# Kernel optimization log

Measured on AMD Instinct MI355X. Metric: run time of the kernel, lower is better.

Reference implementation:

```python
import jax, jax.numpy as jnp
import numpy as np

B, D, H, W, N = 64, 512, 32, 32, 20
E = 512  # emb_size
TEMP = 10.0


def setup_inputs() -> dict:
    key = jax.random.key(0)
    ks = jax.random.split(key, 16)
    inp = {
        "fvisu": jax.random.normal(ks[0], (B, D, H, W), jnp.float32),
        "fword": jax.random.normal(ks[1], (B, N, D), jnp.float32),
        "context_score": jax.random.uniform(ks[2], (B, N), jnp.float32),
        "fcoord": jax.random.normal(ks[3], (B, 8, H, W), jnp.float32),
        "gest": jax.random.normal(ks[4], (B, 8), jnp.float32),
        "word_mask": jax.random.randint(ks[5], (B, N), 0, 2, jnp.int32),
        # parameters (kaiming-uniform-ish scale)
        "attn_map_w": jax.random.normal(ks[6], (E // 2, D), jnp.float32) * (1.0 / np.sqrt(D)),
        "attn_map_b": jnp.zeros((E // 2,), jnp.float32),
        "attn_score_w": jax.random.normal(ks[7], (1, E // 2), jnp.float32) * (1.0 / np.sqrt(E // 2)),
        "attn_score_b": jnp.zeros((1,), jnp.float32),
        "gamma_w": jax.random.normal(ks[8], (2 * E, D), jnp.float32) * (1.0 / np.sqrt(D)),
        "gamma_b": jnp.zeros((2 * E,), jnp.float32),
        "conv1_w": jax.random.normal(ks[9], (E, D + 8), jnp.float32) * (1.0 / np.sqrt(D + 8)),
        "conv1_b": jnp.zeros((E,), jnp.float32),
    }
    return inp


def mask_softmax(attn_score, word_mask, temp=TEMP):
    # score: (B, N)
    score = jax.nn.softmax(attn_score * temp, axis=1)
    m = word_mask.astype(jnp.int32)
    m = m.at[:, 0].set(0)                      # zero CLS position
    idx = jnp.sum(m, axis=1)                   # index of SEP (post-CLS-zeroing), matches torch loop
    m = m.at[jnp.arange(m.shape[0]), idx].set(0)
    ms = score * m.astype(score.dtype)
    return ms / (jnp.sum(ms, axis=1, keepdims=True) + 1e-8)


def reference(fvisu, fword, context_score, fcoord, gest, word_mask,
              attn_map_w, attn_map_b, attn_score_w, attn_score_b,
              gamma_w, gamma_b, conv1_w, conv1_b):
    # fword: (B, N, D) -> module permutes to (B, D, N)
    fw = jnp.transpose(fword, (0, 2, 1))                      # (B, D, N)
    tile_visu = jnp.mean(fvisu.reshape(B, D, -1), axis=2, keepdims=True)  # (B, D, 1)
    context_tile = tile_visu * fw * context_score[:, None, :]  # (B, D, N)

    # 1x1 Conv1d -> GEMM
    attn_feat = jnp.tanh(jnp.einsum('od,bdn->bon', attn_map_w, context_tile)
                         + attn_map_b[None, :, None])          # (B, E/2, N)
    attn_score = (jnp.einsum('oc,bcn->bon', attn_score_w, attn_feat)[:, 0, :]
                  + attn_score_b[0])                           # (B, N)

    mask_score = mask_softmax(attn_score, word_mask)            # (B, N)
    attn_lang = jnp.einsum('bn,bnd->bd', mask_score, fword)     # (B, D)

    # FiLM parameter decode
    film = attn_lang @ gamma_w.T + gamma_b                      # (B, 2E)
    gammas = jnp.tanh(film[:, :E])[:, :, None, None]
    betas = jnp.tanh(film[:, E:])[:, :, None, None]

    # 1x1 Conv2d on concat(fvisu, fcoord) + InstanceNorm2d (no affine, eps=1e-5)
    x = jnp.concatenate([fvisu, fcoord], axis=1)                # (B, D+8, H, W)
    conv = jnp.einsum('oc,bchw->bohw', conv1_w, x) + conv1_b[None, :, None, None]
    mu = jnp.mean(conv, axis=(2, 3), keepdims=True)
    var = jnp.var(conv, axis=(2, 3), keepdims=True)
    norm = (conv - mu) * jax.lax.rsqrt(var + 1e-5)

    fmodu = jax.nn.relu(gammas * norm + betas)
    fmodu = fvisu + fmodu
    return fmodu, attn_lang, attn_score
```

## Files before the change

kernel.cpp:

```cpp
#include <hip/hip_runtime.h>
#include <math.h>

#define BB 64
#define DD 512
#define HW 1024
#define NN 20
#define EE 512
#define CIN 520
#define KCN 17
#define TEMP_F 10.0f

#define OUT_ALANG (BB*DD*HW)
#define OUT_ASCORE (OUT_ALANG + BB*DD)

typedef __bf16 bf16x8 __attribute__((ext_vector_type(8)));
typedef float f32x4 __attribute__((ext_vector_type(4)));

__device__ __forceinline__ unsigned int pack2bf(float a, float b) {
    unsigned int ua = __builtin_bit_cast(unsigned int, a);
    unsigned int ub = __builtin_bit_cast(unsigned int, b);
    ua += 0x7fffu + ((ua >> 16) & 1u);
    ub += 0x7fffu + ((ub >> 16) & 1u);
    return (ua >> 16) | (ub & 0xffff0000u);
}

__device__ __forceinline__ unsigned short bfr(float x) {
    unsigned int u = __builtin_bit_cast(unsigned int, x);
    u += 0x7fffu + ((u >> 16) & 1u);
    return (unsigned short)(u >> 16);
}

__device__ __forceinline__ float bf2f(unsigned short u) {
    unsigned int x = ((unsigned int)u) << 16;
    return __builtin_bit_cast(float, x);
}

__device__ __forceinline__ void glds16(const void* g, void* l) {
    __builtin_amdgcn_global_load_lds(
        (const __attribute__((address_space(1))) void*)g,
        (__attribute__((address_space(3))) void*)l, 16, 0, 0);
}

__global__ __launch_bounds__(256) void k_tilevisu(const float* __restrict__ fvisu,
                                                  float* __restrict__ tv) {
    int row = blockIdx.x;
    const float4* p = (const float4*)(fvisu + (size_t)row * HW);
    int tid = threadIdx.x;
    float4 v = p[tid];
    float s = v.x + v.y + v.z + v.w;
    #pragma unroll
    for (int off = 32; off; off >>= 1) s += __shfl_down(s, off, 64);
    __shared__ float part[4];
    if ((tid & 63) == 0) part[tid >> 6] = s;
    __syncthreads();
    if (tid == 0) tv[row] = (part[0] + part[1] + part[2] + part[3]) * (1.0f / HW);
}

__global__ __launch_bounds__(512) void k_convert_x(
    const float* __restrict__ fvisu, const float* __restrict__ fcoord,
    unsigned short* __restrict__ Xf, float* __restrict__ tv) {
    int L = blockIdx.x;
    int kc = L % KCN;
    int b  = L / KCN;
    int t = threadIdx.x;
    int co = t >> 7;
    int tl = t & 127;
    int cbase = kc * 32 + co * 8;
    float sums[8];
    #pragma unroll
    for (int j = 0; j < 8; ++j) sums[j] = 0.f;

    #pragma unroll
    for (int i = 0; i < 2; ++i) {
        int p0 = (tl + 128 * i) * 4;
        float4 f4[8];
        #pragma unroll
        for (int j = 0; j < 8; ++j) {
            int c = cbase + j;
            if (c < DD) {
                f4[j] = *(const float4*)&fvisu[((size_t)b * DD + c) * HW + p0];
            } else if (c < CIN) {
                f4[j] = *(const float4*)&fcoord[((size_t)b * 8 + (c - DD)) * HW + p0];
            } else {
                f4[j] = make_float4(0.f, 0.f, 0.f, 0.f);
            }
        }
        #pragma unroll
        for (int j = 0; j < 8; ++j)
            if (cbase + j < DD) sums[j] += f4[j].x + f4[j].y + f4[j].z + f4[j].w;

        size_t base = (((size_t)b * 64 + (p0 >> 4)) * KCN + kc) * 512
                    + (size_t)(co * 16 + (p0 & 15)) * 8;
        #pragma unroll
        for (int i2 = 0; i2 < 4; ++i2) {
            uint4 v;
            v.x = pack2bf(((const float*)&f4[0])[i2], ((const float*)&f4[1])[i2]);
            v.y = pack2bf(((const float*)&f4[2])[i2], ((const float*)&f4[3])[i2]);
            v.z = pack2bf(((const float*)&f4[4])[i2], ((const float*)&f4[5])[i2]);
            v.w = pack2bf(((const float*)&f4[6])[i2], ((const float*)&f4[7])[i2]);
            *(uint4*)&Xf[base + (size_t)i2 * 8] = v;
        }
    }

    #pragma unroll
    for (int j = 0; j < 8; ++j) {
        float s = sums[j];
        #pragma unroll
        for (int off = 32; off; off >>= 1) s += __shfl_down(s, off, 64);
        sums[j] = s;
    }
    __shared__ float red[8][8];
    int w = t >> 6;
    if ((t & 63) == 0) {
        #pragma unroll
        for (int j = 0; j < 8; ++j) red[w][j] = sums[j];
    }
    __syncthreads();
    if (t < 32) {
        int j = t & 7, c2 = t >> 3;
        int c = kc * 32 + c2 * 8 + j;
        if (c < DD) tv[(size_t)b * DD + c] = (red[c2 * 2][j] + red[c2 * 2 + 1][j]) * (1.0f / HW);
    }
}

__global__ __launch_bounds__(256) void k_convert_w(
    const float* __restrict__ cw, unsigned short* __restrict__ Wf) {
    int t = threadIdx.x;
    int frag = blockIdx.x * 4 + (t >> 6);
    int l = t & 63;
    int M = frag / KCN, kc = frag % KCN;
    int o = M * 16 + (l & 15);
    int k0 = kc * 32 + (l >> 4) * 8;
    float f[8];
    #pragma unroll
    for (int j = 0; j < 8; ++j) {
        int k = k0 + j;
        f[j] = (k < CIN) ? cw[(size_t)o * CIN + k] : 0.f;
    }
    uint4 v;
    v.x = pack2bf(f[0], f[1]);
    v.y = pack2bf(f[2], f[3]);
    v.z = pack2bf(f[4], f[5]);
    v.w = pack2bf(f[6], f[7]);
    *(uint4*)&Wf[(size_t)frag * 512 + (size_t)l * 8] = v;
}

__global__ __launch_bounds__(256) void k_convert_w2(
    const float* __restrict__ amw, unsigned short* __restrict__ Whi,
    unsigned short* __restrict__ Wlo) {
    int t = threadIdx.x;
    int fid = blockIdx.x * 4 + (t >> 6);
    int l = t & 63;
    int ot = fid >> 4, ks = fid & 15;
    int o = ot * 16 + (l & 15);
    int k0 = ks * 32 + ((l >> 4) & 3) * 8;
    float hi[8], lo[8];
    #pragma unroll
    for (int j = 0; j < 8; ++j) {
        float x = amw[(size_t)o * DD + k0 + j];
        unsigned short h = bfr(x);
        hi[j] = bf2f(h);
        lo[j] = x - hi[j];
    }
    uint4 vh, vl;
    vh.x = pack2bf(hi[0], hi[1]); vh.y = pack2bf(hi[2], hi[3]);
    vh.z = pack2bf(hi[4], hi[5]); vh.w = pack2bf(hi[6], hi[7]);
    vl.x = pack2bf(lo[0], lo[1]); vl.y = pack2bf(lo[2], lo[3]);
    vl.z = pack2bf(lo[4], lo[5]); vl.w = pack2bf(lo[6], lo[7]);
    *(uint4*)&Whi[(size_t)fid * 512 + (size_t)l * 8] = vh;
    *(uint4*)&Wlo[(size_t)fid * 512 + (size_t)l * 8] = vl;
}

__global__ __launch_bounds__(256) void k_attnscore(
    const float* __restrict__ fword, const float* __restrict__ cs,
    const float* __restrict__ tv, const unsigned short* __restrict__ Whi,
    const unsigned short* __restrict__ Wlo, const float* __restrict__ amb,
    const float* __restrict__ asw, const float* __restrict__ asb,
    float* __restrict__ out_ascore) {
    int b = blockIdx.x;
    __shared__ unsigned short uhi[2][16][64][8];
    __shared__ unsigned short ulo[2][16][64][8];
    __shared__ float scoreP[4][32];
    int t = threadIdx.x;

    {
        int n = t & 31, kq = t >> 5;
        float csv = (n < NN) ? cs[b * NN + n] : 0.f;
        const float* fwp = fword + ((size_t)b * NN + (n < NN ? n : 0)) * DD;
        const float* tvp = tv + (size_t)b * DD;
        int mt = n >> 4;
        #pragma unroll
        for (int oc = 0; oc < 8; ++oc) {
            int k = kq * 64 + oc * 8;
            float x[8];
            if (n < NN) {
                float4 f0 = *(const float4*)&fwp[k];
                float4 f1 = *(const float4*)&fwp[k + 4];
                float4 t0 = *(const float4*)&tvp[k];
                float4 t1 = *(const float4*)&tvp[k + 4];
                x[0] = f0.x * t0.x * csv; x[1] = f0.y * t0.y * csv;
                x[2] = f0.z * t0.z * csv; x[3] = f0.w * t0.w * csv;
                x[4] = f1.x * t1.x * csv; x[5] = f1.y * t1.y * csv;
                x[6] = f1.z * t1.z * csv; x[7] = f1.w * t1.w * csv;
            } else {
                #pragma unroll
                for (int j = 0; j < 8; ++j) x[j] = 0.f;
            }
            float h[8], lw[8];
            #pragma unroll
            for (int j = 0; j < 8; ++j) {
                h[j] = bf2f(bfr(x[j]));
                lw[j] = x[j] - h[j];
            }
            int ks = k >> 5;
            int l = (n & 15) + ((k >> 3) & 3) * 16;
            uint4 vh, vl;
            vh.x = pack2bf(h[0], h[1]); vh.y = pack2bf(h[2], h[3]);
            vh.z = pack2bf(h[4], h[5]); vh.w = pack2bf(h[6], h[7]);
            vl.x = pack2bf(lw[0], lw[1]); vl.y = pack2bf(lw[2], lw[3]);
            vl.z = pack2bf(lw[4], lw[5]); vl.w = pack2bf(lw[6], lw[7]);
            *(uint4*)&uhi[mt][ks][l][0] = vh;
            *(uint4*)&ulo[mt][ks][l][0] = vl;
        }
    }
    __syncthreads();

    int w = t >> 6, l = t & 63;
    f32x4 acc[2][4];
    #pragma unroll
    for (int mt = 0; mt < 2; ++mt)
        #pragma unroll
        for (int nt = 0; nt < 4; ++nt) acc[mt][nt] = (f32x4){0.f, 0.f, 0.f, 0.f};

    #pragma unroll 4
    for (int ks = 0; ks < 16; ++ks) {
        bf16x8 ah0 = *(const bf16x8*)&uhi[0][ks][l][0];
        bf16x8 ah1 = *(const bf16x8*)&uhi[1][ks][l][0];
        bf16x8 al0 = *(const bf16x8*)&ulo[0][ks][l][0];
        bf16x8 al1 = *(const bf16x8*)&ulo[1][ks][l][0];
        #pragma unroll
        for (int nt = 0; nt < 4; ++nt) {
            size_t fo = ((size_t)((w * 4 + nt) * 16 + ks)) * 512 + (size_t)l * 8;
            bf16x8 bh = *(const bf16x8*)&Whi[fo];
            bf16x8 bl = *(const bf16x8*)&Wlo[fo];
            acc[0][nt] = __builtin_amdgcn_mfma_f32_16x16x32_bf16(ah0, bh, acc[0][nt], 0, 0, 0);
            acc[0][nt] = __builtin_amdgcn_mfma_f32_16x16x32_bf16(al0, bh, acc[0][nt], 0, 0, 0);
            acc[0][nt] = __builtin_amdgcn_mfma_f32_16x16x32_bf16(ah0, bl, acc[0][nt], 0, 0, 0);
            acc[1][nt] = __builtin_amdgcn_mfma_f32_16x16x32_bf16(ah1, bh, acc[1][nt], 0, 0, 0);
            acc[1][nt] = __builtin_amdgcn_mfma_f32_16x16x32_bf16(al1, bh, acc[1][nt], 0, 0, 0);
            acc[1][nt] = __builtin_amdgcn_mfma_f32_16x16x32_bf16(ah1, bl, acc[1][nt], 0, 0, 0);
        }
    }

    float ambv[4], aswv[4];
    #pragma unroll
    for (int nt = 0; nt < 4; ++nt) {
        int o = (w * 4 + nt) * 16 + (l & 15);
        ambv[nt] = amb[o];
        aswv[nt] = asw[o];
    }
    #pragma unroll
    for (int mt = 0; mt < 2; ++mt) {
        #pragma unroll
        for (int j = 0; j < 4; ++j) {
            float p = 0.f;
            #pragma unroll
            for (int nt = 0; nt < 4; ++nt)
                p += aswv[nt] * tanhf(acc[mt][nt][j] + ambv[nt]);
            #pragma unroll
            for (int off = 1; off < 16; off <<= 1) p += __shfl_xor(p, off, 64);
            if ((l & 15) == 0) scoreP[w][mt * 16 + (l >> 4) * 4 + j] = p;
        }
    }
    __syncthreads();
    if (t < NN)
        out_ascore[b * NN + t] = scoreP[0][t] + scoreP[1][t] + scoreP[2][t] + scoreP[3][t] + asb[0];
}

__global__ __launch_bounds__(256) void k_attnscore_legacy(
    const float* __restrict__ fword, const float* __restrict__ cs,
    const float* __restrict__ tv, const float* __restrict__ amw,
    const float* __restrict__ amb, const float* __restrict__ asw,
    const float* __restrict__ asb, float* __restrict__ out_ascore) {
    int bn = blockIdx.x;
    int b = bn / NN, n = bn % NN;
    __shared__ float u[DD];
    __shared__ float part[4];
    int tid = threadIdx.x;
    float csv = cs[b * NN + n];
    for (int d = tid; d < DD; d += 256)
        u[d] = tv[b * DD + d] * fword[((size_t)b * NN + n) * DD + d] * csv;
    __syncthreads();
    int o = tid;
    const float4* wrow = (const float4*)(amw + (size_t)o * DD);
    const float4* uv = (const float4*)u;
    float dot = 0.f;
    #pragma unroll 4
    for (int i = 0; i < DD / 4; ++i) {
        float4 w4 = wrow[i]; float4 u4 = uv[i];
        dot += w4.x * u4.x + w4.y * u4.y + w4.z * u4.z + w4.w * u4.w;
    }
    float contrib = asw[o] * tanhf(dot + amb[o]);
    #pragma unroll
    for (int off = 32; off; off >>= 1) contrib += __shfl_down(contrib, off, 64);
    if ((tid & 63) == 0) part[tid >> 6] = contrib;
    __syncthreads();
    if (tid == 0) out_ascore[b * NN + n] = part[0] + part[1] + part[2] + part[3] + asb[0];
}

__global__ __launch_bounds__(256) void k_lang_film(
    const float* __restrict__ fword, const int* __restrict__ wmask,
    const float* __restrict__ ascore, const float* __restrict__ gw,
    const float* __restrict__ gb, float* __restrict__ out_alang,
    float* __restrict__ ws_film) {
    int b = blockIdx.x >> 2;
    int qd = blockIdx.x & 3;
    __shared__ float ms[NN];
    __shared__ float al[DD];
    int tid = threadIdx.x;
    if (tid == 0) {
        float s[NN];
        float mx = -1e30f;
        for (int n = 0; n < NN; ++n) { s[n] = ascore[b * NN + n] * TEMP_F; mx = fmaxf(mx, s[n]); }
        float se = 0.f;
        for (int n = 0; n < NN; ++n) { s[n] = expf(s[n] - mx); se += s[n]; }
        int m[NN]; int idx = 0;
        for (int n = 0; n < NN; ++n) m[n] = wmask[b * NN + n];
        m[0] = 0;
        for (int n = 0; n < NN; ++n) idx += m[n];
        m[idx] = 0;
        float tot = 0.f;
        for (int n = 0; n < NN; ++n) { float v = (s[n] / se) * (float)m[n]; ms[n] = v; tot += v; }
        float inv = 1.f / (tot + 1e-8f);
        for (int n = 0; n < NN; ++n) ms[n] *= inv;
    }
    __syncthreads();
    for (int d = tid; d < DD; d += 256) {
        float a = 0.f;
        #pragma unroll
        for (int n = 0; n < NN; ++n) a += ms[n] * fword[((size_t)b * NN + n) * DD + d];
        al[d] = a;
        if (qd == 0) out_alang[b * DD + d] = a;
    }
    __syncthreads();
    {
        int r = qd * 256 + tid;
        const float4* grow = (const float4*)(gw + (size_t)r * DD);
        const float4* av = (const float4*)al;
        float dot = 0.f;
        #pragma unroll 4
        for (int i = 0; i < DD / 4; ++i) {
            float4 g4 = grow[i]; float4 a4 = av[i];
            dot += g4.x * a4.x + g4.y * a4.y + g4.z * a4.z + g4.w * a4.w;
        }
        ws_film[b * 2 * EE + r] = tanhf(dot + gb[r]);
    }
}

__global__ __launch_bounds__(512, 2) void k_gemm_in_film(
    const unsigned short* __restrict__ Xf, const unsigned short* __restrict__ Wf,
    const float* __restrict__ film, float* __restrict__ out) {
    __shared__ __align__(16) unsigned char lds[136192];
    int L = blockIdx.x;
    int r = L & 63, ot = L >> 6;
    int b = ((r >> 3) & 7) * 8 + (r & 7);
    int t = threadIdx.x;
    int w = t >> 6, l = t & 63;

    unsigned char* slot0 = lds + w * 16384;
    unsigned char* slot1 = slot0 + 8192;
    const unsigned short* Xw = Xf + ((size_t)b * 64 + w * 8) * (KCN * 512);
    const unsigned short* Wb = Wf + (size_t)(ot * 4) * (KCN * 512);
    int ot2 = 2 * ot;

    f32x4 acc[4][8];
    #pragma unroll
    for (int m = 0; m < 4; ++m)
        #pragma unroll
        for (int n = 0; n < 8; ++n) acc[m][n] = (f32x4){0.f, 0.f, 0.f, 0.f};

    auto kcof = [&](int j) -> int {
        if (j < 15) return j + (j >= ot2 ? 2 : 0);
        return (j == 15) ? ot2 : (ot2 + 1);
    };
    auto issue = [&](int j) {
        int kc = kcof(j);
        unsigned char* s = (j & 1) ? slot1 : slot0;
        #pragma unroll
        for (int i = 0; i < 8; ++i)
            glds16((const void*)(Xw + ((size_t)i * KCN + kc) * 512 + (size_t)l * 8),
                   s + i * 1024);
    };
    auto loadA = [&](int j, bf16x8* af) {
        int kc = kcof(j);
        #pragma unroll
        for (int m = 0; m < 4; ++m)
            af[m] = *(const bf16x8*)(Wb + ((size_t)m * KCN + kc) * 512 + (size_t)l * 8);
    };

    bf16x8 afA[4], afB[4];
    issue(0);
    loadA(0, afA);

    #pragma unroll
    for (int j = 0; j < KCN; ++j) {
        if (j < KCN - 1) {
            issue(j + 1);
            if (j & 1) loadA(j + 1, afA); else loadA(j + 1, afB);
            asm volatile("s_waitcnt vmcnt(12)" ::: "memory");
        } else {
            asm volatile("s_waitcnt vmcnt(0)" ::: "memory");
        }
        __builtin_amdgcn_sched_barrier(0);
        const unsigned char* s = (j & 1) ? slot1 : slot0;
        bf16x8 bfr[8];
        #pragma unroll
        for (int n = 0; n < 8; ++n)
            bfr[n] = *(const bf16x8*)(s + n * 1024 + l * 16);
        __builtin_amdgcn_s_setprio(1);
        #pragma unroll
        for (int m = 0; m < 4; ++m) {
            const bf16x8 a = (j & 1) ? afB[m] : afA[m];
            #pragma unroll
            for (int n = 0; n < 8; ++n)
                acc[m][n] = __builtin_amdgcn_mfma_f32_16x16x32_bf16(a, bfr[n], acc[m][n], 0, 0, 0);
        }
        __builtin_amdgcn_s_setprio(0);
    }

    float* sP = (float*)(lds + 131072);
    float* qP = sP + 512;
    float* st = qP + 512;
    #pragma unroll
    for (int m = 0; m < 4; ++m) {
        #pragma unroll
        for (int j = 0; j < 4; ++j) {
            float s = 0.f, q = 0.f;
            #pragma unroll
            for (int n = 0; n < 8; ++n) { float v = acc[m][n][j]; s += v; q += v * v; }
            #pragma unroll
            for (int off = 1; off < 16; off <<= 1) {
                s += __shfl_xor(s, off, 64);
                q += __shfl_xor(q, off, 64);
            }
            if ((l & 15) == 0) {
                int ol = m * 16 + (l >> 4) * 4 + j;
                sP[w * 64 + ol] = s;
                qP[w * 64 + ol] = q;
            }
        }
    }
    __syncthreads();
    if (t < 64) {
        float s = 0.f, q = 0.f;
        #pragma unroll
        for (int ww = 0; ww < 8; ++ww) { s += sP[ww * 64 + t]; q += qP[ww * 64 + t]; }
        float mu = s * (1.0f / HW);
        float var = q * (1.0f / HW) - mu * mu;
        int oc = ot * 64 + t;
        st[t * 4 + 0] = mu;
        st[t * 4 + 1] = rsqrtf(var + 1e-5f);
        st[t * 4 + 2] = film[b * 1024 + oc];
        st[t * 4 + 3] = film[b * 1024 + 512 + oc];
    }
    __syncthreads();

    float* ob = out + ((size_t)b * DD + ot * 64) * HW;
    int q4 = l >> 4;
    #pragma unroll
    for (int m = 0; m < 4; ++m) {
        const unsigned char* rsl = (m < 2) ? slot1 : slot0;
        int lp = ((m & 1) * 2 + (q4 >> 1)) * 16 + (l & 15);
        int off8 = (q4 & 1) * 8;
        #pragma unroll
        for (int n = 0; n < 8; ++n) {
            ushort4 rb = *(const ushort4*)(rsl + n * 1024 + lp * 16 + off8);
            int px = w * 128 + n * 16 + (l & 15);
            #pragma unroll
            for (int jj = 0; jj < 4; ++jj) {
                int ol = m * 16 + q4 * 4 + jj;
                f32x4 sv = *(const f32x4*)&st[ol * 4];
                float nrm = (acc[m][n][jj] - sv[0]) * sv[1];
                float rr = sv[2] * nrm + sv[3];
                rr = rr > 0.f ? rr : 0.f;
                float res = bf2f(((const unsigned short*)&rb)[jj]);
                ob[(size_t)ol * HW + px] = res + rr;
            }
        }
    }
}

__global__ __launch_bounds__(256) void k_conv_in_film(
    const float* __restrict__ fvisu, const float* __restrict__ fcoord,
    const float* __restrict__ cw, const float* __restrict__ film,
    float* __restrict__ out) {
    int L = blockIdx.x;
    int b = L & 63;
    int tgt = L >> 6;
    int o0 = tgt * 16;
    int tid = threadIdx.x;
    __shared__ float xs[8][HW];
    __shared__ float red[16][4][2];
    __shared__ float stats[16][2];
    float acc[16][4];
    #pragma unroll
    for (int o = 0; o < 16; ++o)
        #pragma unroll
        for (int j = 0; j < 4; ++j) acc[o][j] = 0.f;

    const float* xb_v = fvisu + (size_t)b * DD * HW;
    const float* xb_c = fcoord + (size_t)b * 8 * HW;

    for (int c0 = 0; c0 < CIN; c0 += 8) {
        #pragma unroll
        for (int i = 0; i < 8; ++i) {
            int c = c0 + i;
            const float* src = (c < DD) ? (xb_v + (size_t)c * HW) : (xb_c + (size_t)(c - DD) * HW);
            ((float4*)xs[i])[tid] = ((const float4*)src)[tid];
        }
        __syncthreads();
        #pragma unroll
        for (int i = 0; i < 8; ++i) {
            float xv[4];
            #pragma unroll
            for (int j = 0; j < 4; ++j) xv[j] = xs[i][tid + 256 * j];
            #pragma unroll
            for (int o = 0; o < 16; ++o) {
                float wv = cw[(size_t)(o0 + o) * CIN + (c0 + i)];
                #pragma unroll
                for (int j = 0; j < 4; ++j) acc[o][j] = fmaf(wv, xv[j], acc[o][j]);
            }
        }
        __syncthreads();
    }
    int lane = tid & 63, wid = tid >> 6;
    #pragma unroll
    for (int o = 0; o < 16; ++o) {
        float s = 0.f, q = 0.f;
        #pragma unroll
        for (int j = 0; j < 4; ++j) { s += acc[o][j]; q += acc[o][j] * acc[o][j]; }
        #pragma unroll
        for (int off = 32; off; off >>= 1) {
            s += __shfl_down(s, off, 64);
            q += __shfl_down(q, off, 64);
        }
        if (lane == 0) { red[o][wid][0] = s; red[o][wid][1] = q; }
    }
    __syncthreads();
    if (tid < 16) {
        float s = red[tid][0][0] + red[tid][1][0] + red[tid][2][0] + red[tid][3][0];
        float q = red[tid][0][1] + red[tid][1][1] + red[tid][2][1] + red[tid][3][1];
        float mu = s * (1.0f / HW);
        float var = q * (1.0f / HW) - mu * mu;
        stats[tid][0] = mu;
        stats[tid][1] = rsqrtf(var + 1e-5f);
    }
    __syncthreads();
    #pragma unroll
    for (int o = 0; o < 16; ++o) {
        int oc = o0 + o;
        float mu = stats[o][0], rs = stats[o][1];
        float g  = film[b * 1024 + oc];
        float be = film[b * 1024 + 512 + oc];
        const float* fv = xb_v + (size_t)oc * HW;
        float* op = out + ((size_t)b * DD + oc) * HW;
        #pragma unroll
        for (int j = 0; j < 4; ++j) {
            int p = tid + 256 * j;
            float nrm = (acc[o][j] - mu) * rs;
            float rr = g * nrm + be;
            rr = rr > 0.f ? rr : 0.f;
            op[p] = fv[p] + rr;
        }
    }
}

extern "C" void kernel_launch(void* const* d_in, const int* in_sizes, int n_in,
                              void* d_out, int out_size, void* d_ws, size_t ws_size,
                              hipStream_t stream) {
    const float* fvisu  = (const float*)d_in[0];
    const float* fword  = (const float*)d_in[1];
    const float* cscore = (const float*)d_in[2];
    const float* fcoord = (const float*)d_in[3];
    const int*   wmask  = (const int*)d_in[5];
    const float* amw    = (const float*)d_in[6];
    const float* amb    = (const float*)d_in[7];
    const float* asw    = (const float*)d_in[8];
    const float* asb    = (const float*)d_in[9];
    const float* gw     = (const float*)d_in[10];
    const float* gb     = (const float*)d_in[11];
    const float* cw     = (const float*)d_in[12];

    float* out = (float*)d_out;
    float* ws_tv   = (float*)d_ws;
    float* ws_film = ws_tv + BB * DD;
    unsigned short* Xf  = (unsigned short*)((char*)d_ws + 393216);
    unsigned short* Wf  = (unsigned short*)((char*)d_ws + 393216 + 71303168);
    unsigned short* Whi = (unsigned short*)((char*)d_ws + 393216 + 71303168 + 557056);
    unsigned short* Wlo = Whi + 256 * 512;
    const size_t need = 393216 + 71303168 + 557056 + 524288;

    float* out_alang  = out + OUT_ALANG;
    float* out_ascore = out + OUT_ASCORE;

    if (ws_size >= need) {
        k_convert_w<<<136, 256, 0, stream>>>(cw, Wf);
        k_convert_w2<<<64, 256, 0, stream>>>(amw, Whi, Wlo);
        k_convert_x<<<BB * KCN, 512, 0, stream>>>(fvisu, fcoord, Xf, ws_tv);
        k_attnscore<<<BB, 256, 0, stream>>>(fword, cscore, ws_tv, Whi, Wlo, amb, asw, asb, out_ascore);
        k_lang_film<<<BB * 4, 256, 0, stream>>>(fword, wmask, out_ascore, gw, gb, out_alang, ws_film);
        k_gemm_in_film<<<512, 512, 0, stream>>>(Xf, Wf, ws_film, out);
    } else {
        k_tilevisu<<<BB * DD, 256, 0, stream>>>(fvisu, ws_tv);
        k_attnscore_legacy<<<BB * NN, 256, 0, stream>>>(fword, cscore, ws_tv, amw, amb, asw, asb, out_ascore);
        k_lang_film<<<BB * 4, 256, 0, stream>>>(fword, wmask, out_ascore, gw, gb, out_alang, ws_film);
        k_conv_in_film<<<BB * 32, 256, 0, stream>>>(fvisu, fcoord, cw, ws_film, out);
    }
}
```

Measured before the change: 179.9 us.

## Load GEMM B fragments straight to registers instead of staging through LDS

The fused conv+InstanceNorm+FiLM GEMM kernel no longer stages the X tiles through a 136KB LDS buffer with global-to-LDS loads. It double-buffers both A and B fragments directly in registers. The residual fvisu values used in the epilogue are now re-read from global memory instead of the LDS slots. This shrinks LDS use, which could allow more resident blocks, but it raises register pressure, drops the explicit vmcnt pipelining and adds extra global reads in the epilogue.

```diff
diff --git a/kernel.cpp b/kernel.cpp
--- a/kernel.cpp
+++ b/kernel.cpp
@@ -360,17 +360,17 @@
 __global__ __launch_bounds__(512, 2) void k_gemm_in_film(
     const unsigned short* __restrict__ Xf, const unsigned short* __restrict__ Wf,
     const float* __restrict__ film, float* __restrict__ out) {
-    __shared__ __align__(16) unsigned char lds[136192];
+    __shared__ float sP[8][64];
+    __shared__ float qP[8][64];
+    __shared__ float st[64][4];
     int L = blockIdx.x;
     int r = L & 63, ot = L >> 6;
     int b = ((r >> 3) & 7) * 8 + (r & 7);
     int t = threadIdx.x;
     int w = t >> 6, l = t & 63;
 
-    unsigned char* slot0 = lds + w * 16384;
-    unsigned char* slot1 = slot0 + 8192;
-    const unsigned short* Xw = Xf + ((size_t)b * 64 + w * 8) * (KCN * 512);
-    const unsigned short* Wb = Wf + (size_t)(ot * 4) * (KCN * 512);
+    const unsigned short* Xw = Xf + ((size_t)b * 64 + w * 8) * (KCN * 512) + (size_t)l * 8;
+    const unsigned short* Wb = Wf + (size_t)(ot * 4) * (KCN * 512) + (size_t)l * 8;
     int ot2 = 2 * ot;
 
     f32x4 acc[4][8];
@@ -383,54 +383,43 @@
         if (j < 15) return j + (j >= ot2 ? 2 : 0);
         return (j == 15) ? ot2 : (ot2 + 1);
     };
-    auto issue = [&](int j) {
+    auto loadB = [&](int j, bf16x8* bf_) {
         int kc = kcof(j);
-        unsigned char* s = (j & 1) ? slot1 : slot0;
         #pragma unroll
         for (int i = 0; i < 8; ++i)
-            glds16((const void*)(Xw + ((size_t)i * KCN + kc) * 512 + (size_t)l * 8),
-                   s + i * 1024);
+            bf_[i] = *(const bf16x8*)(Xw + ((size_t)i * KCN + kc) * 512);
     };
     auto loadA = [&](int j, bf16x8* af) {
         int kc = kcof(j);
         #pragma unroll
         for (int m = 0; m < 4; ++m)
-            af[m] = *(const bf16x8*)(Wb + ((size_t)m * KCN + kc) * 512 + (size_t)l * 8);
+            af[m] = *(const bf16x8*)(Wb + ((size_t)m * KCN + kc) * 512);
     };
-
-    bf16x8 afA[4], afB[4];
-    issue(0);
-    loadA(0, afA);
+    auto compute = [&](const bf16x8* af, const bf16x8* bf_) {
+        __builtin_amdgcn_s_setprio(1);
+        #pragma unroll
+        for (int m = 0; m < 4; ++m)
+            #pragma unroll
+            for (int n = 0; n < 8; ++n)
+                acc[m][n] = __builtin_amdgcn_mfma_f32_16x16x32_bf16(af[m], bf_[n], acc[m][n], 0, 0, 0);
+        __builtin_amdgcn_s_setprio(0);
+    };
+
+    bf16x8 bA[8], bB[8], aA[4], aB[4];
+    loadB(0, bA);
+    loadA(0, aA);
 
     #pragma unroll
     for (int j = 0; j < KCN; ++j) {
-        if (j < KCN - 1) {
-            issue(j + 1);
-            if (j & 1) loadA(j + 1, afA); else loadA(j + 1, afB);
-            asm volatile("s_waitcnt vmcnt(12)" ::: "memory");
+        if (j & 1) {
+            if (j + 1 < KCN) { loadB(j + 1, bA); loadA(j + 1, aA); }
+            compute(aB, bB);
         } else {
-            asm volatile("s_waitcnt vmcnt(0)" ::: "memory");
-        }
-        __builtin_amdgcn_sched_barrier(0);
-        const unsigned char* s = (j & 1) ? slot1 : slot0;
-        bf16x8 bfr[8];
-        #pragma unroll
-        for (int n = 0; n < 8; ++n)
-            bfr[n] = *(const bf16x8*)(s + n * 1024 + l * 16);
-        __builtin_amdgcn_s_setprio(1);
-        #pragma unroll
-        for (int m = 0; m < 4; ++m) {
-            const bf16x8 a = (j & 1) ? afB[m] : afA[m];
-            #pragma unroll
-            for (int n = 0; n < 8; ++n)
-                acc[m][n] = __builtin_amdgcn_mfma_f32_16x16x32_bf16(a, bfr[n], acc[m][n], 0, 0, 0);
-        }
-        __builtin_amdgcn_s_setprio(0);
-    }
-
-    float* sP = (float*)(lds + 131072);
-    float* qP = sP + 512;
-    float* st = qP + 512;
+            if (j + 1 < KCN) { loadB(j + 1, bB); loadA(j + 1, aB); }
+            compute(aA, bA);
+        }
+    }
+
     #pragma unroll
     for (int m = 0; m < 4; ++m) {
         #pragma unroll
@@ -445,8 +434,8 @@
             }
             if ((l & 15) == 0) {
                 int ol = m * 16 + (l >> 4) * 4 + j;
-                sP[w * 64 + ol] = s;
-                qP[w * 64 + ol] = q;
+                sP[w][ol] = s;
+                qP[w][ol] = q;
             }
         }
     }
@@ -454,14 +443,14 @@
     if (t < 64) {
         float s = 0.f, q = 0.f;
         #pragma unroll
-        for (int ww = 0; ww < 8; ++ww) { s += sP[ww * 64 + t]; q += qP[ww * 64 + t]; }
+        for (int ww = 0; ww < 8; ++ww) { s += sP[ww][t]; q += qP[ww][t]; }
         float mu = s * (1.0f / HW);
         float var = q * (1.0f / HW) - mu * mu;
         int oc = ot * 64 + t;
-        st[t * 4 + 0] = mu;
-        st[t * 4 + 1] = rsqrtf(var + 1e-5f);
-        st[t * 4 + 2] = film[b * 1024 + oc];
-        st[t * 4 + 3] = film[b * 1024 + 512 + oc];
+        st[t][0] = mu;
+        st[t][1] = rsqrtf(var + 1e-5f);
+        st[t][2] = film[b * 1024 + oc];
+        st[t][3] = film[b * 1024 + 512 + oc];
     }
     __syncthreads();
 
@@ -469,17 +458,18 @@
     int q4 = l >> 4;
     #pragma unroll
     for (int m = 0; m < 4; ++m) {
-        const unsigned char* rsl = (m < 2) ? slot1 : slot0;
+        int kc_m = ot2 + (m >> 1);
         int lp = ((m & 1) * 2 + (q4 >> 1)) * 16 + (l & 15);
-        int off8 = (q4 & 1) * 8;
+        int uo = lp * 8 + (q4 & 1) * 4;
         #pragma unroll
         for (int n = 0; n < 8; ++n) {
-            ushort4 rb = *(const ushort4*)(rsl + n * 1024 + lp * 16 + off8);
+            ushort4 rb = *(const ushort4*)(Xf + ((size_t)b * 64 + w * 8 + n) * (KCN * 512)
+                                           + ((size_t)kc_m) * 512 + uo);
             int px = w * 128 + n * 16 + (l & 15);
             #pragma unroll
             for (int jj = 0; jj < 4; ++jj) {
                 int ol = m * 16 + q4 * 4 + jj;
-                f32x4 sv = *(const f32x4*)&st[ol * 4];
+                f32x4 sv = *(const f32x4*)&st[ol][0];
                 float nrm = (acc[m][n][jj] - sv[0]) * sv[1];
                 float rr = sv[2] * nrm + sv[3];
                 rr = rr > 0.f ? rr : 0.f;
```

After: 183.2 us. About the same (+1.8%).
